# Optimization experiments

Hardware: AMD Instinct MI355X
Metric: run time of the kernel (lower is better)

The kernel has to match this reference:

```python
import jax, jax.numpy as jnp
import numpy as np

T, IN, HID, OUT, B = 256, 1024, 1024, 1024, 128


def setup_inputs() -> dict:
    key = jax.random.key(0)
    k1, k2, k3, k4 = jax.random.split(key, 4)
    return {
        "inputs": jax.random.normal(k1, (T, IN, B), dtype=jnp.float32),
        "h_prev": jnp.zeros((HID, B), dtype=jnp.float32),
        "Wxh": jax.random.normal(k2, (HID, IN), dtype=jnp.float32) * 0.01,
        "Whh": jax.random.normal(k3, (HID, HID), dtype=jnp.float32) * 0.01,
        "Why": jax.random.normal(k4, (OUT, HID), dtype=jnp.float32) * 0.01,
        "bh": jnp.zeros((HID, 1), dtype=jnp.float32),
        "by": jnp.zeros((OUT, 1), dtype=jnp.float32),
    }


def reference(inputs, h_prev, Wxh, Whh, Why, bh, by):
    # inputs: [T, IN, B]; h: [HID, B]
    def step(h, x):
        h = jnp.tanh(Wxh @ x + Whh @ h + bh)
        y = Why @ h + by
        return h, y

    h_final, ys = jax.lax.scan(step, h_prev, inputs)
    return ys, h_final  # ys: [T, OUT, B], h_final: [HID, B]
```

## Files before the change

### kernel.cpp

```cpp
#include <hip/hip_runtime.h>
#include <cmath>

#define T_STEPS 256
#define DIN  1024
#define DHID 1024
#define DOUT 1024
#define NB   128
#define BH   (DHID*NB)

typedef unsigned short u16;
typedef unsigned int   u32;
typedef unsigned long long u64;
typedef __attribute__((ext_vector_type(8))) __bf16 bf16x8;
typedef __attribute__((ext_vector_type(4))) float  f32x4;

__device__ __forceinline__ u16 f2bf(float f){
  u32 u = __builtin_bit_cast(u32, f);
  u32 r = (u + 0x7fffu + ((u >> 16) & 1u)) >> 16;
  return (u16)r;
}
__device__ __forceinline__ float bf2f(u16 h){
  u32 u = ((u32)h) << 16;
  return __builtin_bit_cast(float, u);
}

__device__ __forceinline__ void st_agent_u16(u16* p, u16 v){
  __hip_atomic_store(p, v, __ATOMIC_RELAXED, __HIP_MEMORY_SCOPE_AGENT);
}
__device__ __forceinline__ u64 ld_agent_u64(const u64* p){
  return __hip_atomic_load(p, __ATOMIC_RELAXED, __HIP_MEMORY_SCOPE_AGENT);
}

__global__ __launch_bounds__(256) void wconv(const float* __restrict__ w0,
                                             const float* __restrict__ w1,
                                             const float* __restrict__ w2,
                                             u16* __restrict__ dst){
  const int idx = blockIdx.x*256 + threadIdx.x;
  const int seg = idx >> 18;
  const int off = idx & 262143;
  const float* src = seg==0 ? w0 : (seg==1 ? w1 : w2);
  const float4 v = ((const float4*)src)[off];
  ushort4 o = make_ushort4(f2bf(v.x), f2bf(v.y), f2bf(v.z), f2bf(v.w));
  ((ushort4*)dst)[idx] = o;
}

__global__ __launch_bounds__(256) void hprevT(const float* __restrict__ hp,
                                              u16* __restrict__ HT0){
  const int tid = blockIdx.x*256 + threadIdx.x;
  const int b = tid >> 10, m = tid & 1023;
  HT0[tid] = f2bf(hp[(size_t)m*NB + b]);
}

__global__ __launch_bounds__(256) void xT_k(const float* __restrict__ x,
                                            u16* __restrict__ xt){
  __shared__ float tile[64][65];
  const int t  = blockIdx.z;
  const int k0 = blockIdx.y*64;
  const int b0 = blockIdx.x*64;
  const int tx = threadIdx.x & 63, ty = threadIdx.x >> 6;
  const float* src = x + (size_t)t*DIN*NB + (size_t)k0*NB + b0;
#pragma unroll
  for(int r=0;r<16;r++){ int k = r*4 + ty; tile[k][tx] = src[(size_t)k*NB + tx]; }
  __syncthreads();
  u16* dst = xt + (size_t)t*NB*DIN + (size_t)b0*DIN + k0;
#pragma unroll
  for(int r=0;r<16;r++){ int b = r*4 + ty; dst[(size_t)b*DIN + tx] = f2bf(tile[tx][b]); }
}

__global__ __launch_bounds__(256) void gemm_xw(const u16* __restrict__ XT,
                                               const u16* __restrict__ WxB,
                                               const float* __restrict__ bh,
                                               u16* __restrict__ AT){
  const int t  = blockIdx.y;
  const int mj = blockIdx.x;
  __shared__ __align__(16) u16 As[128*40];
  __shared__ __align__(16) u16 Bs[128*40];
  const u16* aG = XT + (size_t)t*NB*DIN;
  const u16* bG = WxB + (size_t)mj*128*DIN;
  const int tid = threadIdx.x;
  const int lane = tid & 63, w = tid >> 6;
  const int wr = (w & 1)*64, wc = (w >> 1)*64;
  const int l15 = lane & 15, q = lane >> 4;
  const int sr = tid >> 2;
  const int sk = (tid & 3)*8;

  f32x4 acc[4][4] = {};
  uint4 pa0 = *(const uint4*)&aG[(size_t)sr*DIN + sk];
  uint4 pa1 = *(const uint4*)&aG[(size_t)(sr+64)*DIN + sk];
  uint4 pb0 = *(const uint4*)&bG[(size_t)sr*DIN + sk];
  uint4 pb1 = *(const uint4*)&bG[(size_t)(sr+64)*DIN + sk];

  for(int it = 0; it < DIN/32; ++it){
    __syncthreads();
    *(uint4*)&As[sr*40 + sk]      = pa0;
    *(uint4*)&As[(sr+64)*40 + sk] = pa1;
    *(uint4*)&Bs[sr*40 + sk]      = pb0;
    *(uint4*)&Bs[(sr+64)*40 + sk] = pb1;
    __syncthreads();
    if(it < DIN/32 - 1){
      const int k0 = (it+1)*32;
      pa0 = *(const uint4*)&aG[(size_t)sr*DIN + k0 + sk];
      pa1 = *(const uint4*)&aG[(size_t)(sr+64)*DIN + k0 + sk];
      pb0 = *(const uint4*)&bG[(size_t)sr*DIN + k0 + sk];
      pb1 = *(const uint4*)&bG[(size_t)(sr+64)*DIN + k0 + sk];
    }
    bf16x8 af[4], bf[4];
#pragma unroll
    for(int i=0;i<4;i++) af[i] = *(const bf16x8*)&As[(wr + i*16 + l15)*40 + q*8];
#pragma unroll
    for(int j=0;j<4;j++) bf[j] = *(const bf16x8*)&Bs[(wc + j*16 + l15)*40 + q*8];
#pragma unroll
    for(int i=0;i<4;i++)
#pragma unroll
      for(int j=0;j<4;j++)
        acc[i][j] = __builtin_amdgcn_mfma_f32_16x16x32_bf16(af[i], bf[j], acc[i][j], 0,0,0);
  }

  u16* out = AT + (size_t)t*NB*DHID;
#pragma unroll
  for(int j=0;j<4;j++){
    const int mg = mj*128 + wc + j*16 + l15;
    const float bhv = bh[mg];
#pragma unroll
    for(int i=0;i<4;i++){
#pragma unroll
      for(int r=0;r<4;r++){
        const int bg = wr + i*16 + q*4 + r;
        out[(size_t)bg*DHID + mg] = f2bf(acc[i][j][r] + bhv);
      }
    }
  }
}

#define RSTEP_BLOCKS 64
__global__ __launch_bounds__(512, 1) void rnn_steps(const u16* __restrict__ WhB,
                                                    const u16* __restrict__ AT,
                                                    u16* __restrict__ HT,
                                                    u32* bar){
  const int mslice = blockIdx.x & 7;
  const int bg     = blockIdx.x >> 3;
  __shared__ __align__(16) u16 Hs[16*1032];
  const int tid = threadIdx.x;
  const int lane = tid & 63, w = tid >> 6;
  const int l15 = lane & 15, q = lane >> 4, q8 = q*8;
  const int mw = mslice*128 + w*16;

  bf16x8 wf[32];
  { const u16* wsrc = WhB + (size_t)(mw + l15)*DHID;
#pragma unroll
    for(int i=0;i<32;i++) wf[i] = *(const bf16x8*)&wsrc[i*32 + q8];
  }

  const int hr  = tid >> 5;
  const int hc  = tid & 31;

  for(int t=0; t<T_STEPS; ++t){
    const u64* Hp64 = (const u64*)(HT + (size_t)t*BH + (size_t)(bg*16 + hr)*DHID) + hc;

    u64 hv[8];
#pragma unroll
    for(int i=0;i<8;i++) hv[i] = ld_agent_u64(Hp64 + i*32);

    const u16* At = AT + (size_t)t*BH;
    u16 aval[4];
#pragma unroll
    for(int r=0;r<4;r++)
      aval[r] = At[(size_t)(bg*16 + q*4 + r)*DHID + mw + l15];

    u64* hs64 = (u64*)&Hs[hr*1032] + hc;
#pragma unroll
    for(int i=0;i<8;i++) hs64[i*32] = hv[i];
    __syncthreads();

    f32x4 acc = {0.f,0.f,0.f,0.f};
#pragma unroll
    for(int kk=0;kk<32;kk++){
      bf16x8 a = *(const bf16x8*)&Hs[l15*1032 + kk*32 + q8];
      acc = __builtin_amdgcn_mfma_f32_16x16x32_bf16(a, wf[kk], acc, 0,0,0);
    }

    u16* Hn = HT + (size_t)(t+1)*BH;
#pragma unroll
    for(int r=0;r<4;r++){
      float v = acc[r] + bf2f(aval[r]);
      st_agent_u16(&Hn[(size_t)(bg*16 + q*4 + r)*DHID + mw + l15], f2bf(tanhf(v)));
    }

    if(t < T_STEPS-1){
      asm volatile("s_waitcnt vmcnt(0)" ::: "memory");
      __syncthreads();
      if(tid == 0){
        __hip_atomic_fetch_add(bar, 1u, __ATOMIC_RELAXED, __HIP_MEMORY_SCOPE_AGENT);
        const u32 tgt = (u32)(t+1)*RSTEP_BLOCKS;
        while(__hip_atomic_load(bar, __ATOMIC_RELAXED, __HIP_MEMORY_SCOPE_AGENT) < tgt)
          __builtin_amdgcn_s_sleep(2);
      }
      __syncthreads();
    }
  }
}

__global__ __launch_bounds__(256) void gemm_hy(const u16* __restrict__ WyB,
                                               const u16* __restrict__ HT,
                                               const float* __restrict__ by,
                                               float* __restrict__ Y){
  const int t  = blockIdx.y;
  const int mi = blockIdx.x;
  __shared__ __align__(16) u16 As[128*40];
  __shared__ __align__(16) u16 Bs[128*40];
  const u16* aG = WyB + (size_t)mi*128*DHID;
  const u16* bG = HT  + (size_t)(t+1)*BH;
  const int tid = threadIdx.x;
  const int lane = tid & 63, w = tid >> 6;
  const int wr = (w & 1)*64, wc = (w >> 1)*64;
  const int l15 = lane & 15, q = lane >> 4;
  const int sr = tid >> 2;
  const int sk = (tid & 3)*8;

  f32x4 acc[4][4] = {};
  uint4 pa0 = *(const uint4*)&aG[(size_t)sr*DHID + sk];
  uint4 pa1 = *(const uint4*)&aG[(size_t)(sr+64)*DHID + sk];
  uint4 pb0 = *(const uint4*)&bG[(size_t)sr*DHID + sk];
  uint4 pb1 = *(const uint4*)&bG[(size_t)(sr+64)*DHID + sk];

  for(int it = 0; it < DHID/32; ++it){
    __syncthreads();
    *(uint4*)&As[sr*40 + sk]      = pa0;
    *(uint4*)&As[(sr+64)*40 + sk] = pa1;
    *(uint4*)&Bs[sr*40 + sk]      = pb0;
    *(uint4*)&Bs[(sr+64)*40 + sk] = pb1;
    __syncthreads();
    if(it < DHID/32 - 1){
      const int k0 = (it+1)*32;
      pa0 = *(const uint4*)&aG[(size_t)sr*DHID + k0 + sk];
      pa1 = *(const uint4*)&aG[(size_t)(sr+64)*DHID + k0 + sk];
      pb0 = *(const uint4*)&bG[(size_t)sr*DHID + k0 + sk];
      pb1 = *(const uint4*)&bG[(size_t)(sr+64)*DHID + k0 + sk];
    }
    bf16x8 af[4], bf[4];
#pragma unroll
    for(int i=0;i<4;i++) af[i] = *(const bf16x8*)&As[(wr + i*16 + l15)*40 + q*8];
#pragma unroll
    for(int j=0;j<4;j++) bf[j] = *(const bf16x8*)&Bs[(wc + j*16 + l15)*40 + q*8];
#pragma unroll
    for(int i=0;i<4;i++)
#pragma unroll
      for(int j=0;j<4;j++)
        acc[i][j] = __builtin_amdgcn_mfma_f32_16x16x32_bf16(af[i], bf[j], acc[i][j], 0,0,0);
  }

  float* out = Y + (size_t)t*DOUT*NB;
#pragma unroll
  for(int i=0;i<4;i++){
#pragma unroll
    for(int r=0;r<4;r++){
      const int og = mi*128 + wr + i*16 + q*4 + r;
      const float byv = by[og];
#pragma unroll
      for(int j=0;j<4;j++){
        const int bg = wc + j*16 + l15;
        out[(size_t)og*NB + bg] = acc[i][j][r] + byv;
      }
    }
  }
}

__global__ __launch_bounds__(256) void hfinal(const u16* __restrict__ HT,
                                              float* __restrict__ dst){
  const int tid = blockIdx.x*256 + threadIdx.x;
  const int m = tid >> 7, b = tid & 127;
  dst[tid] = bf2f(HT[(size_t)T_STEPS*BH + (size_t)b*DHID + m]);
}

extern "C" void kernel_launch(void* const* d_in, const int* in_sizes, int n_in,
                              void* d_out, int out_size, void* d_ws, size_t ws_size,
                              hipStream_t stream)
{
  const float* x   = (const float*)d_in[0];
  const float* hp  = (const float*)d_in[1];
  const float* wxh = (const float*)d_in[2];
  const float* whh = (const float*)d_in[3];
  const float* why = (const float*)d_in[4];
  const float* bh  = (const float*)d_in[5];
  const float* by  = (const float*)d_in[6];
  float* out = (float*)d_out;

  u16* WxB = (u16*)d_ws;
  u16* WhB = WxB + (size_t)1024*1024;
  u16* WyB = WhB + (size_t)1024*1024;
  u16* HT  = WyB + (size_t)1024*1024;
  u32* bar = (u32*)(HT + (size_t)(T_STEPS+1)*BH);

  u16* XT = (u16*)d_out;
  u16* AT = XT + (size_t)T_STEPS*NB*DIN;

  wconv  <<<3072, 256, 0, stream>>>(wxh, whh, why, WxB);
  hprevT <<<512,  256, 0, stream>>>(hp, HT);
  xT_k   <<<dim3(2,16,T_STEPS), 256, 0, stream>>>(x, XT);
  gemm_xw<<<dim3(8,T_STEPS),    256, 0, stream>>>(XT, WxB, bh, AT);
  hipMemsetAsync(bar, 0, 64, stream);
  rnn_steps<<<RSTEP_BLOCKS, 512, 0, stream>>>(WhB, AT, HT, bar);
  gemm_hy<<<dim3(8,T_STEPS), 256, 0, stream>>>(WyB, HT, by, out);
  hfinal <<<512, 256, 0, stream>>>(HT, out + (size_t)T_STEPS*DOUT*NB);
}
```

Before: 1.500 ms.

## Replace global atomic barrier with per-group flags and widen per-warp tiles

The recurrent step kernel now runs 256 threads per block, and each wave computes two 16-column tiles. Each wave holds 64 weight fragments in registers, and the K loop is split into even and odd accumulators to give the MFMA chain more independent work. New hidden values are staged through shared memory so they go out as 64-bit stores instead of scattered 16-bit atomics. The single global counter barrier is replaced by per-block flags, so each block waits only on the 8 m-slices of its own batch group. This cuts contention on every step, but it relies on cross-block visibility through relaxed agent-scope operations and adds register pressure.

```diff
diff --git a/kernel.cpp b/kernel.cpp
--- a/kernel.cpp
+++ b/kernel.cpp
@@ -24,11 +24,11 @@
   return __builtin_bit_cast(float, u);
 }
 
-__device__ __forceinline__ void st_agent_u16(u16* p, u16 v){
-  __hip_atomic_store(p, v, __ATOMIC_RELAXED, __HIP_MEMORY_SCOPE_AGENT);
-}
 __device__ __forceinline__ u64 ld_agent_u64(const u64* p){
   return __hip_atomic_load(p, __ATOMIC_RELAXED, __HIP_MEMORY_SCOPE_AGENT);
+}
+__device__ __forceinline__ void st_agent_u64(u64* p, u64 v){
+  __hip_atomic_store(p, v, __ATOMIC_RELAXED, __HIP_MEMORY_SCOPE_AGENT);
 }
 
 __global__ __launch_bounds__(256) void wconv(const float* __restrict__ w0,
@@ -133,67 +133,89 @@
 }
 
 #define RSTEP_BLOCKS 64
-__global__ __launch_bounds__(512, 1) void rnn_steps(const u16* __restrict__ WhB,
+__global__ __launch_bounds__(256, 1) void rnn_steps(const u16* __restrict__ WhB,
                                                     const u16* __restrict__ AT,
                                                     u16* __restrict__ HT,
-                                                    u32* bar){
+                                                    u32* __restrict__ flags){
   const int mslice = blockIdx.x & 7;
   const int bg     = blockIdx.x >> 3;
   __shared__ __align__(16) u16 Hs[16*1032];
+  __shared__ __align__(16) u16 Es[4*16*40];
   const int tid = threadIdx.x;
   const int lane = tid & 63, w = tid >> 6;
   const int l15 = lane & 15, q = lane >> 4, q8 = q*8;
-  const int mw = mslice*128 + w*16;
-
-  bf16x8 wf[32];
-  { const u16* wsrc = WhB + (size_t)(mw + l15)*DHID;
-#pragma unroll
-    for(int i=0;i<32;i++) wf[i] = *(const bf16x8*)&wsrc[i*32 + q8];
-  }
-
-  const int hr  = tid >> 5;
-  const int hc  = tid & 31;
+  const int mw = mslice*128 + w*32;
+
+  bf16x8 wf0[32], wf1[32];
+  { const u16* ws0 = WhB + (size_t)(mw + l15)*DHID;
+    const u16* ws1 = WhB + (size_t)(mw + 16 + l15)*DHID;
+#pragma unroll
+    for(int i=0;i<32;i++){ wf0[i] = *(const bf16x8*)&ws0[i*32 + q8];
+                           wf1[i] = *(const bf16x8*)&ws1[i*32 + q8]; }
+  }
+
+  const int hr = tid >> 4;
+  const int hc = tid & 15;
+  const int eb = lane >> 2, ec = lane & 3;
 
   for(int t=0; t<T_STEPS; ++t){
     const u64* Hp64 = (const u64*)(HT + (size_t)t*BH + (size_t)(bg*16 + hr)*DHID) + hc;
 
-    u64 hv[8];
-#pragma unroll
-    for(int i=0;i<8;i++) hv[i] = ld_agent_u64(Hp64 + i*32);
+    u64 hv[16];
+#pragma unroll
+    for(int i=0;i<16;i++) hv[i] = ld_agent_u64(Hp64 + i*16);
 
     const u16* At = AT + (size_t)t*BH;
-    u16 aval[4];
-#pragma unroll
-    for(int r=0;r<4;r++)
-      aval[r] = At[(size_t)(bg*16 + q*4 + r)*DHID + mw + l15];
+    u16 aval[2][4];
+#pragma unroll
+    for(int h=0;h<2;h++)
+#pragma unroll
+      for(int r=0;r<4;r++)
+        aval[h][r] = At[(size_t)(bg*16 + q*4 + r)*DHID + mw + h*16 + l15];
 
     u64* hs64 = (u64*)&Hs[hr*1032] + hc;
 #pragma unroll
-    for(int i=0;i<8;i++) hs64[i*32] = hv[i];
-    __syncthreads();
-
-    f32x4 acc = {0.f,0.f,0.f,0.f};
-#pragma unroll
-    for(int kk=0;kk<32;kk++){
-      bf16x8 a = *(const bf16x8*)&Hs[l15*1032 + kk*32 + q8];
-      acc = __builtin_amdgcn_mfma_f32_16x16x32_bf16(a, wf[kk], acc, 0,0,0);
-    }
-
-    u16* Hn = HT + (size_t)(t+1)*BH;
+    for(int i=0;i<16;i++) hs64[i*16] = hv[i];
+    __syncthreads();
+
+    f32x4 a0e = {0,0,0,0}, a0o = {0,0,0,0}, a1e = {0,0,0,0}, a1o = {0,0,0,0};
+#pragma unroll
+    for(int kk=0;kk<32;kk+=2){
+      bf16x8 ae = *(const bf16x8*)&Hs[l15*1032 + kk*32 + q8];
+      bf16x8 ao = *(const bf16x8*)&Hs[l15*1032 + (kk+1)*32 + q8];
+      a0e = __builtin_amdgcn_mfma_f32_16x16x32_bf16(ae, wf0[kk],   a0e, 0,0,0);
+      a1e = __builtin_amdgcn_mfma_f32_16x16x32_bf16(ae, wf1[kk],   a1e, 0,0,0);
+      a0o = __builtin_amdgcn_mfma_f32_16x16x32_bf16(ao, wf0[kk+1], a0o, 0,0,0);
+      a1o = __builtin_amdgcn_mfma_f32_16x16x32_bf16(ao, wf1[kk+1], a1o, 0,0,0);
+    }
+    f32x4 acc0 = a0e + a0o, acc1 = a1e + a1o;
+
+    u16* Ew = Es + w*640;
 #pragma unroll
     for(int r=0;r<4;r++){
-      float v = acc[r] + bf2f(aval[r]);
-      st_agent_u16(&Hn[(size_t)(bg*16 + q*4 + r)*DHID + mw + l15], f2bf(tanhf(v)));
-    }
+      float v0 = acc0[r] + bf2f(aval[0][r]);
+      float v1 = acc1[r] + bf2f(aval[1][r]);
+      Ew[(q*4+r)*40 + l15]      = f2bf(tanhf(v0));
+      Ew[(q*4+r)*40 + 16 + l15] = f2bf(tanhf(v1));
+    }
+    __syncthreads();
+    u64 h0 = *(const u64*)&Ew[eb*40 + ec*8];
+    u64 h1 = *(const u64*)&Ew[eb*40 + ec*8 + 4];
+    u64* Hn = (u64*)(HT + (size_t)(t+1)*BH + (size_t)(bg*16 + eb)*DHID + mw + ec*8);
+    st_agent_u64(Hn,     h0);
+    st_agent_u64(Hn + 1, h1);
+
+    asm volatile("s_waitcnt vmcnt(0)" ::: "memory");
 
     if(t < T_STEPS-1){
-      asm volatile("s_waitcnt vmcnt(0)" ::: "memory");
       __syncthreads();
-      if(tid == 0){
-        __hip_atomic_fetch_add(bar, 1u, __ATOMIC_RELAXED, __HIP_MEMORY_SCOPE_AGENT);
-        const u32 tgt = (u32)(t+1)*RSTEP_BLOCKS;
-        while(__hip_atomic_load(bar, __ATOMIC_RELAXED, __HIP_MEMORY_SCOPE_AGENT) < tgt)
-          __builtin_amdgcn_s_sleep(2);
+      if(tid == 0)
+        __hip_atomic_store(&flags[(size_t)(bg*8 + mslice)*32], (u32)(t+1),
+                           __ATOMIC_RELAXED, __HIP_MEMORY_SCOPE_AGENT);
+      if(tid < 8){
+        while(__hip_atomic_load(&flags[(size_t)(bg*8 + tid)*32],
+                                __ATOMIC_RELAXED, __HIP_MEMORY_SCOPE_AGENT) < (u32)(t+1))
+          ;
       }
       __syncthreads();
     }
@@ -289,7 +311,7 @@
   u16* WhB = WxB + (size_t)1024*1024;
   u16* WyB = WhB + (size_t)1024*1024;
   u16* HT  = WyB + (size_t)1024*1024;
-  u32* bar = (u32*)(HT + (size_t)(T_STEPS+1)*BH);
+  u32* flags = (u32*)(HT + (size_t)(T_STEPS+1)*BH);
 
   u16* XT = (u16*)d_out;
   u16* AT = XT + (size_t)T_STEPS*NB*DIN;
@@ -298,8 +320,8 @@
   hprevT <<<512,  256, 0, stream>>>(hp, HT);
   xT_k   <<<dim3(2,16,T_STEPS), 256, 0, stream>>>(x, XT);
   gemm_xw<<<dim3(8,T_STEPS),    256, 0, stream>>>(XT, WxB, bh, AT);
-  hipMemsetAsync(bar, 0, 64, stream);
-  rnn_steps<<<RSTEP_BLOCKS, 512, 0, stream>>>(WhB, AT, HT, bar);
+  (void)hipMemsetAsync(flags, 0, 8192, stream);
+  rnn_steps<<<RSTEP_BLOCKS, 256, 0, stream>>>(WhB, AT, HT, flags);
   gemm_hy<<<dim3(8,T_STEPS), 256, 0, stream>>>(WyB, HT, by, out);
   hfinal <<<512, 256, 0, stream>>>(HT, out + (size_t)T_STEPS*DOUT*NB);
 }
```

New measurement: 1.446 ms. 1.04x faster.
